# Kernel tuning notes

Measured on AMD Instinct MI355X. Metric: run time of the kernel, lower is better.

## Reference

```python
import jax, jax.numpy as jnp
import numpy as np

B, L, D_MODEL = 2, 1024, 512
N_LAYERS = 4
D_INNER = 2 * D_MODEL          # expand=2
D_STATE = 16
D_CONV = 4
DT_RANK = D_MODEL // 16        # ceil(512/16)=32
EPS = 1e-5


def layernorm(x, w, b):
    m = jnp.mean(x, axis=-1, keepdims=True)
    v = jnp.var(x, axis=-1, keepdims=True)
    return (x - m) * jax.lax.rsqrt(v + EPS) * w + b


def selective_scan(u, delta, A, Bm, Cm, Dp):
    # u, delta: [b,l,d]; Bm, Cm: [b,l,n]; A: [d,n]; Dp: [d]
    def step(h, inp):
        dt_t, b_t, c_t, u_t = inp            # [b,d],[b,n],[b,n],[b,d]
        dA = jnp.exp(dt_t[:, :, None] * A)   # [b,d,n]
        h = dA * h + (dt_t * u_t)[:, :, None] * b_t[:, None, :]
        y = jnp.einsum('bdn,bn->bd', h, c_t)
        return h, y

    b, l, d = u.shape
    n = A.shape[1]
    h0 = jnp.zeros((b, d, n), u.dtype)
    xs = (jnp.swapaxes(delta, 0, 1), jnp.swapaxes(Bm, 0, 1),
          jnp.swapaxes(Cm, 0, 1), jnp.swapaxes(u, 0, 1))
    _, ys = jax.lax.scan(step, h0, xs)       # ys: [l,b,d]
    return jnp.swapaxes(ys, 0, 1) + u * Dp


def mamba(x, in_w, conv_w, conv_b, xp_w, dtp_w, dtp_b, A_log, Dp, out_w):
    # x: [b,l,D_MODEL]
    xz = x @ in_w.T                          # [b,l,2*d_inner]
    xc, z = jnp.split(xz, 2, axis=-1)
    xc = jnp.swapaxes(xc, 1, 2)              # [b,d_inner,l]
    xc = jax.lax.conv_general_dilated(
        xc, conv_w[:, None, :], (1,), [(D_CONV - 1, 0)],
        feature_group_count=D_INNER,
        dimension_numbers=('NCH', 'OIH', 'NCH')) + conv_b[None, :, None]
    xc = jax.nn.silu(jnp.swapaxes(xc, 1, 2))  # [b,l,d_inner]
    x_dbl = xc @ xp_w.T                       # [b,l,dt_rank+2n]
    dt = x_dbl[..., :DT_RANK]
    Bm = x_dbl[..., DT_RANK:DT_RANK + D_STATE]
    Cm = x_dbl[..., DT_RANK + D_STATE:]
    dt = jax.nn.softplus(dt @ dtp_w.T + dtp_b)
    A = -jnp.exp(A_log)
    y = selective_scan(xc, dt, A, Bm, Cm, Dp)
    y = y * jax.nn.silu(z)
    return y @ out_w.T


def forward(x, in_proj_w, conv_w, conv_b, x_proj_w, dt_proj_w, dt_proj_b,
            A_log, D_param, out_proj_w, ln_w, ln_b, fnorm_w, fnorm_b):
    residual = None
    for i in range(in_proj_w.shape[0]):
        residual = x if residual is None else x + residual
        xn = layernorm(x, ln_w[i], ln_b[i])  # norm of incoming x (as in torch src)
        h1 = mamba(xn, in_proj_w[i, 0], conv_w[i, 0], conv_b[i, 0],
                   x_proj_w[i, 0], dt_proj_w[i, 0], dt_proj_b[i, 0],
                   A_log[i, 0], D_param[i, 0], out_proj_w[i, 0])
        h2 = mamba(jnp.flip(xn, axis=1), in_proj_w[i, 1], conv_w[i, 1],
                   conv_b[i, 1], x_proj_w[i, 1], dt_proj_w[i, 1],
                   dt_proj_b[i, 1], A_log[i, 1], D_param[i, 1],
                   out_proj_w[i, 1])
        x = h1 + h2                           # bi_add: NOT flipped back, faithful
    x = x + residual
    return layernorm(x, fnorm_w, fnorm_b)


def setup_inputs() -> dict:
    key = jax.random.key(0)
    ks = jax.random.split(key, 8)
    P2 = (N_LAYERS, 2)
    inp = {}
    inp['x'] = jax.random.normal(ks[0], (B, L, D_MODEL), jnp.float32)
    inp['in_proj_w'] = jax.random.normal(ks[1], P2 + (2 * D_INNER, D_MODEL), jnp.float32) * 0.02
    inp['conv_w'] = jax.random.normal(ks[2], P2 + (D_INNER, D_CONV), jnp.float32) * 0.1
    inp['conv_b'] = jnp.zeros(P2 + (D_INNER,), jnp.float32)
    inp['x_proj_w'] = jax.random.normal(ks[3], P2 + (DT_RANK + 2 * D_STATE, D_INNER), jnp.float32) * 0.02
    inp['dt_proj_w'] = jax.random.normal(ks[4], P2 + (D_INNER, DT_RANK), jnp.float32) * (DT_RANK ** -0.5)
    inp['dt_proj_b'] = jnp.full(P2 + (D_INNER,), float(np.log(np.expm1(0.01))), jnp.float32)
    inp['A_log'] = jnp.broadcast_to(jnp.log(jnp.arange(1, D_STATE + 1, dtype=jnp.float32)), P2 + (D_INNER, D_STATE)).copy()
    inp['D_param'] = jnp.ones(P2 + (D_INNER,), jnp.float32)
    inp['out_proj_w'] = jax.random.normal(ks[5], P2 + (D_MODEL, D_INNER), jnp.float32) * 0.02
    inp['ln_w'] = jnp.ones((N_LAYERS, D_MODEL), jnp.float32)
    inp['ln_b'] = jnp.zeros((N_LAYERS, D_MODEL), jnp.float32)
    inp['fnorm_w'] = jnp.ones((D_MODEL,), jnp.float32)
    inp['fnorm_b'] = jnp.zeros((D_MODEL,), jnp.float32)
    return inp


def reference(x, in_proj_w, conv_w, conv_b, x_proj_w, dt_proj_w, dt_proj_b,
              A_log, D_param, out_proj_w, ln_w, ln_b, fnorm_w, fnorm_b):
    return forward(x, in_proj_w, conv_w, conv_b, x_proj_w, dt_proj_w,
                   dt_proj_b, A_log, D_param, out_proj_w, ln_w, ln_b,
                   fnorm_w, fnorm_b)
```

## Files before the change

kernel.cpp:

```cpp
#include <hip/hip_runtime.h>
#include <hip/hip_bf16.h>
#include <type_traits>

#define B_   2
#define L_   1024
#define DM   512
#define DI   1024
#define DS   16
#define DTR  32
#define ROWS (B_*L_)
#define NCH  16
#define CHUNK (L_/NCH)

#define PO_CW    0
#define PO_CB    32768
#define PO_XPW   40960
#define PO_DTW   565248
#define PO_DTB   827392
#define PO_ALOG  835584
#define PO_DP    966656
#define PO_LNW   974848
#define PO_LNB   976896
#define PO_FNW   978944
#define PO_FNB   979456
#define PO_END   979968

typedef __bf16 bf16x8 __attribute__((ext_vector_type(8)));
typedef float  f32x4  __attribute__((ext_vector_type(4)));
using bf16 = __hip_bfloat16;

__device__ __forceinline__ bf16x8 ld8(const bf16* p){
    return *reinterpret_cast<const bf16x8*>(p);
}
__device__ __forceinline__ float b2f(bf16 v){ return __bfloat162float(v); }

__device__ __forceinline__ void async_cp16(const bf16* g, bf16* s){
    __builtin_amdgcn_global_load_lds(
        (const __attribute__((address_space(1))) unsigned int*)g,
        (__attribute__((address_space(3))) unsigned int*)s, 16, 0, 0);
}

__global__ void detect_kernel(const void* Dp_raw, int* flag){
    *flag = (*(const unsigned int*)Dp_raw == 0x3F800000u) ? 1 : 0;
}

__device__ __forceinline__ bf16 cvload(const void* s, long o, int f){
    return f ? __float2bfloat16(((const float*)s)[o]) : ((const bf16*)s)[o];
}

__global__ void cvt_kernel(const void* src, long off, bf16* dst, int n,
                           const int* flag){
    int i = blockIdx.x*256 + threadIdx.x;
    if (i < n) dst[i] = cvload(src, off + i, *flag);
}

__global__ void cvt_wout_kernel(const void* src, long loff, bf16* dst,
                                const int* flag){
    int i = blockIdx.x*256 + threadIdx.x;
    if (i >= 512*2048) return;
    int n = i >> 11, rest = i & 2047, dir = rest >> 10, d = rest & 1023;
    long o = loff + ((long)dir*512 + n)*1024 + d;
    dst[i] = cvload(src, o, *flag);
}

__global__ void cvt_params_kernel(const void* cw, const void* cb, const void* xpw,
                                  const void* dtw, const void* dtb, const void* al,
                                  const void* dp, const void* lnw, const void* lnb,
                                  const void* fnw, const void* fnb,
                                  bf16* dst, const int* flag){
    int i = blockIdx.x*256 + threadIdx.x;
    if (i >= PO_END) return;
    int f = *flag;
    const void* s; long o;
    if      (i < PO_CB)   { s = cw;  o = i; }
    else if (i < PO_XPW)  { s = cb;  o = i - PO_CB; }
    else if (i < PO_DTW)  { s = xpw; o = i - PO_XPW; }
    else if (i < PO_DTB)  { s = dtw; o = i - PO_DTW; }
    else if (i < PO_ALOG) { s = dtb; o = i - PO_DTB; }
    else if (i < PO_DP)   { s = al;  o = i - PO_ALOG; }
    else if (i < PO_LNW)  { s = dp;  o = i - PO_DP; }
    else if (i < PO_LNB)  { s = lnw; o = i - PO_LNW; }
    else if (i < PO_FNW)  { s = lnb; o = i - PO_LNB; }
    else if (i < PO_FNB)  { s = fnw; o = i - PO_FNW; }
    else                  { s = fnb; o = i - PO_FNB; }
    dst[i] = cvload(s, o, f);
}

__global__ void init_kernel(const void* xin, float* __restrict__ X,
                            float* __restrict__ R, const int* flag){
    size_t i = (size_t)blockIdx.x*256 + threadIdx.x;
    X[i] = *flag ? ((const float*)xin)[i] : b2f(((const bf16*)xin)[i]);
    R[i] = 0.f;
}

__global__ void ln_kernel(const float* __restrict__ X, float* __restrict__ R,
                          const bf16* __restrict__ w, const bf16* __restrict__ b,
                          void* __restrict__ out, int mode, const int* flag){
    int row = blockIdx.x, lane = threadIdx.x;
    size_t base = (size_t)row*DM + lane*8;
    float v[8];
    *(float4*)&v[0] = *(const float4*)(X+base);
    *(float4*)&v[4] = *(const float4*)(X+base+4);
    if (mode == 0){
        float4 r0 = *(const float4*)(R+base);
        float4 r1 = *(const float4*)(R+base+4);
        r0.x += v[0]; r0.y += v[1]; r0.z += v[2]; r0.w += v[3];
        r1.x += v[4]; r1.y += v[5]; r1.z += v[6]; r1.w += v[7];
        *(float4*)(R+base)   = r0;
        *(float4*)(R+base+4) = r1;
    } else {
        float4 r0 = *(const float4*)(R+base);
        float4 r1 = *(const float4*)(R+base+4);
        v[0]+=r0.x; v[1]+=r0.y; v[2]+=r0.z; v[3]+=r0.w;
        v[4]+=r1.x; v[5]+=r1.y; v[6]+=r1.z; v[7]+=r1.w;
    }
    float s=0.f, sq=0.f;
    #pragma unroll
    for (int j=0;j<8;++j){ s += v[j]; sq += v[j]*v[j]; }
    #pragma unroll
    for (int off=32; off>=1; off>>=1){
        s  += __shfl_xor(s,  off, 64);
        sq += __shfl_xor(sq, off, 64);
    }
    float mean = s*(1.f/DM);
    float var  = sq*(1.f/DM) - mean*mean;
    float rs   = rsqrtf(var + 1e-5f);
    bf16x8 wv = ld8(w + lane*8), bv = ld8(b + lane*8);
    float res[8];
    #pragma unroll
    for (int j=0;j<8;++j)
        res[j] = (v[j]-mean)*rs*(float)wv[j] + (float)bv[j];
    if (mode == 1 && *flag){
        float* of = (float*)out;
        *(float4*)(of+base)   = make_float4(res[0],res[1],res[2],res[3]);
        *(float4*)(of+base+4) = make_float4(res[4],res[5],res[6],res[7]);
    } else {
        union { bf16 h[8]; uint4 u; } o;
        #pragma unroll
        for (int j=0;j<8;++j) o.h[j] = __float2bfloat16(res[j]);
        *(uint4*)((bf16*)out + base) = o.u;
    }
}

template<int WM, int WN, int SK, typename CT>
__global__ __launch_bounds__(WM*WN*64)
void gemm_lds(const bf16* __restrict__ A, const bf16* __restrict__ W,
              CT* __restrict__ C, int K, int lda, int ldw, int ldc,
              int selTiles, long wSel){
    constexpr int BM = WM*64, BN = WN*64, T = WM*WN*64;
    constexpr int RA = (BM*4)/T, RB = (BN*4)/T;
    __shared__ __align__(16) bf16 sA[BM*32];
    __shared__ __align__(16) bf16 sB[BN*32];
    int tid = threadIdx.x;
    int mtile = blockIdx.y, ntile = blockIdx.x;
    if (mtile >= selTiles) W += wSel;
    int m0 = mtile*BM, n0 = ntile*BN;
    int kPer = K/SK, kBeg = blockIdx.z*kPer, kEnd = kBeg + kPer;
    if (SK > 1)
        C += (size_t)blockIdx.z * (size_t)(gridDim.y*BM) * (size_t)(gridDim.x*BN);
    int wave = tid>>6, lane = tid&63, quad = lane>>4, r = lane&15;
    int wrow = wave / WN, wcol = wave % WN;
    const bf16* Abase = A + (size_t)m0*lda;
    const bf16* Wbase = W + (size_t)n0*ldw;
    f32x4 acc[4][4] = {};
    for (int k0 = kBeg; k0 < kEnd; k0 += 32){
        #pragma unroll
        for (int rr=0; rr<RA; ++rr){
            int q = rr*T + tid;
            async_cp16(Abase + (size_t)(q>>2)*lda + k0 + (q&3)*8, &sA[q*8]);
        }
        #pragma unroll
        for (int rr=0; rr<RB; ++rr){
            int q = rr*T + tid;
            async_cp16(Wbase + (size_t)(q>>2)*ldw + k0 + (q&3)*8, &sB[q*8]);
        }
        __syncthreads();
        bf16x8 af[4], bw[4];
        #pragma unroll
        for (int mt=0; mt<4; ++mt)
            af[mt] = *(const bf16x8*)&sA[(wrow*64 + mt*16 + r)*32 + quad*8];
        #pragma unroll
        for (int nt=0; nt<4; ++nt)
            bw[nt] = *(const bf16x8*)&sB[(wcol*64 + nt*16 + r)*32 + quad*8];
        #pragma unroll
        for (int mt=0; mt<4; ++mt)
            #pragma unroll
            for (int nt=0; nt<4; ++nt)
                acc[mt][nt] = __builtin_amdgcn_mfma_f32_16x16x32_bf16(
                    af[mt], bw[nt], acc[mt][nt], 0,0,0);
        __syncthreads();
    }
    #pragma unroll
    for (int mt=0; mt<4; ++mt){
        #pragma unroll
        for (int nt=0; nt<4; ++nt){
            int col = n0 + wcol*64 + nt*16 + r;
            #pragma unroll
            for (int ri=0; ri<4; ++ri){
                int row = m0 + wrow*64 + mt*16 + quad*4 + ri;
                size_t idx = (size_t)row*ldc + col;
                if constexpr (std::is_same<CT, bf16>::value)
                    C[idx] = __float2bfloat16(acc[mt][nt][ri]);
                else
                    C[idx] = acc[mt][nt][ri];
            }
        }
    }
}

__global__ void reduce_out(const float* __restrict__ P, float* __restrict__ X){
    int i = blockIdx.x*256 + threadIdx.x;
    X[i] = (P[i] + P[i+1048576]) + (P[i+2097152] + P[i+3145728]);
}

__global__ void reduce_xd(const float* __restrict__ P, float* __restrict__ XD){
    int i = blockIdx.x*256 + threadIdx.x;
    float s = 0.f;
    #pragma unroll
    for (int k=0;k<8;++k) s += P[k*262144 + i];
    int j = i & 63, grow = i >> 6, dir = grow >> 11, row = grow & 2047;
    XD[row*128 + dir*64 + j] = s;
}

__global__ void conv_kernel(const bf16* __restrict__ XZ, const bf16* __restrict__ cw,
                            const bf16* __restrict__ cb, bf16* __restrict__ XC){
    int id  = blockIdx.x*256 + threadIdx.x;
    int d   = id & (DI-1);
    int t   = (id >> 10) & (L_-1);
    int b   = (id >> 20) & 1;
    int dir = id >> 21;
    float wv[4];
    #pragma unroll
    for (int k=0;k<4;++k) wv[k] = b2f(cw[((size_t)dir*DI + d)*4 + k]);
    float acc = b2f(cb[dir*DI + d]);
    #pragma unroll
    for (int k=0;k<4;++k){
        int tau = t - 3 + k;
        if (tau >= 0){
            int sig = dir ? (L_-1-tau) : tau;
            acc += wv[k] * b2f(XZ[((size_t)(b*L_ + sig))*4096 + dir*2048 + d]);
        }
    }
    float s = acc * (1.f/(1.f + __expf(-acc)));
    XC[((size_t)dir*ROWS + (size_t)b*L_ + t)*DI + d] = __float2bfloat16(s);
}

__global__ void dtproj_kernel(const float* __restrict__ XD, const bf16* __restrict__ dtw,
                              const bf16* __restrict__ dtb, bf16* __restrict__ DT){
    int id  = blockIdx.x*256 + threadIdx.x;
    int d   = id & (DI-1);
    int row = (id >> 10) & (ROWS-1);
    int dir = id >> 21;
    const float* xr = XD + (size_t)row*128 + dir*64;
    const bf16*  wp = dtw + ((size_t)dir*DI + d)*DTR;
    float acc = b2f(dtb[dir*DI + d]);
    #pragma unroll
    for (int kk=0;kk<4;++kk){
        bf16x8 wv = ld8(wp + kk*8);
        #pragma unroll
        for (int j=0;j<8;++j) acc += xr[kk*8+j]*(float)wv[j];
    }
    float sp = acc > 20.f ? acc : log1pf(__expf(acc));
    DT[((size_t)dir*ROWS + row)*DI + d] = __float2bfloat16(sp);
}

template<int PHASE>
__global__ __launch_bounds__(256)
void scan_phase(const bf16* __restrict__ DT, const bf16* __restrict__ XC,
                const float* __restrict__ XD, const bf16* __restrict__ XZ,
                const bf16* __restrict__ Al, const bf16* __restrict__ Dp,
                float* __restrict__ SP, float* __restrict__ SH,
                bf16* __restrict__ Y){
    int dirb = blockIdx.z, dir = dirb >> 1, b = dirb & 1;
    int c    = blockIdx.y;
    int d0   = blockIdx.x*128;
    int tid  = threadIdx.x;
    int dl   = tid >> 1, nh = tid & 1;
    int d    = d0 + dl;

    __shared__ bf16  sDT[CHUNK][128];
    __shared__ bf16  sW [CHUNK][128];
    __shared__ float sBC[CHUNK][32];
    __shared__ bf16  sExtra[(PHASE==3) ? CHUNK*128*2 : 2];
    bf16* sG   = &sExtra[0];
    bf16* sUDG = &sExtra[CHUNK*128];

    #pragma unroll
    for (int it=0; it<2; ++it){
        int idx = it*256 + tid;
        int t = idx >> 3, j = idx & 7;
        const float* src = XD + ((size_t)(b*L_) + c*CHUNK + t)*128 + dir*64 + 32 + j*4;
        *(float4*)&sBC[t][j*4] = *(const float4*)src;
    }
    {
        int dcol = tid & 127;
        float Dval = (PHASE==3) ? b2f(Dp[dir*DI + d0 + dcol]) : 0.f;
        #pragma unroll 8
        for (int it=0; it<32; ++it){
            int idx = it*256 + tid;
            int t = idx >> 7;
            int tg = c*CHUNK + t;
            size_t row = (size_t)b*L_ + tg;
            size_t gidx = ((size_t)dir*ROWS + row)*DI + d0 + dcol;
            float dt = b2f(DT[gidx]);
            float u  = b2f(XC[gidx]);
            sDT[t][dcol] = __float2bfloat16(dt);
            sW [t][dcol] = __float2bfloat16(dt*u);
            if (PHASE == 3){
                size_t zrow = dir ? ((size_t)b*L_ + (L_-1-tg)) : row;
                float zv = b2f(XZ[zrow*4096 + dir*2048 + 1024 + d0 + dcol]);
                float g  = zv*(1.f/(1.f + __expf(-zv)));
                sG[t*128 + dcol]   = __float2bfloat16(g);
                sUDG[t*128 + dcol] = __float2bfloat16(u*Dval*g);
            }
        }
    }

    float An[8];
    {
        const bf16* ap = Al + ((size_t)dir*DI + d)*DS + nh*8;
        bf16x8 av = ld8(ap);
        #pragma unroll
        for (int j=0;j<8;++j) An[j] = -__expf((float)av[j]);
    }
    __syncthreads();

    float h[8], pr[8];
    size_t so = ((size_t)(dirb*NCH + c)*DI + d)*DS + nh*8;
    if (PHASE == 3){
        *(f32x4*)&h[0] = *(const f32x4*)&SH[so];
        *(f32x4*)&h[4] = *(const f32x4*)&SH[so+4];
    } else {
        #pragma unroll
        for (int j=0;j<8;++j){ h[j]=0.f; pr[j]=1.f; }
    }

    bf16* Yp = Y + ((size_t)b*L_ + c*CHUNK)*2048 + dir*DI + d;

    for (int tl=0; tl<CHUNK; ++tl){
        float dtv = b2f(sDT[tl][dl]);
        float wv  = b2f(sW [tl][dl]);
        const float* Bp = &sBC[tl][nh*8];
        float y = 0.f;
        #pragma unroll
        for (int j=0;j<8;++j){
            float dA = __expf(dtv*An[j]);
            h[j] = dA*h[j] + wv*Bp[j];
            if (PHASE == 1) pr[j] *= dA;
            else            y += h[j]*Bp[16+j];
        }
        if (PHASE == 3){
            y += __shfl_xor(y, 1, 64);
            if (nh == 0){
                float g   = b2f(sG[tl*128 + dl]);
                float udg = b2f(sUDG[tl*128 + dl]);
                Yp[(size_t)tl*2048] = __float2bfloat16(y*g + udg);
            }
        }
    }
    if (PHASE == 1){
        *(f32x4*)&SP[so]   = *(f32x4*)&pr[0];
        *(f32x4*)&SP[so+4] = *(f32x4*)&pr[4];
        *(f32x4*)&SH[so]   = *(f32x4*)&h[0];
        *(f32x4*)&SH[so+4] = *(f32x4*)&h[4];
    }
}

__global__ void scan_combine(const float* __restrict__ SP, float* __restrict__ SH){
    int id   = blockIdx.x*256 + threadIdx.x;
    int dn   = id & (DI*DS - 1);
    int dirb = id >> 14;
    float hp = 0.f;
    for (int c=0;c<NCH;++c){
        size_t o = ((size_t)(dirb*NCH + c)*DI*DS) + dn;
        float pp = SP[o], he = SH[o];
        float nh = pp*hp + he;
        SH[o] = hp;
        hp = nh;
    }
}

extern "C" void kernel_launch(void* const* d_in, const int* in_sizes, int n_in,
                              void* d_out, int out_size, void* d_ws, size_t ws_size,
                              hipStream_t stream){
    const void* x_raw    = d_in[0];
    const void* inw_raw  = d_in[1];
    const void* convw_raw= d_in[2];
    const void* convb_raw= d_in[3];
    const void* xpw_raw  = d_in[4];
    const void* dtw_raw  = d_in[5];
    const void* dtb_raw  = d_in[6];
    const void* alog_raw = d_in[7];
    const void* dp_raw   = d_in[8];
    const void* outw_raw = d_in[9];
    const void* lnw_raw  = d_in[10];
    const void* lnb_raw  = d_in[11];
    const void* fnw_raw  = d_in[12];
    const void* fnb_raw  = d_in[13];

    char* ws = (char*)d_ws;
    float* X   = (float*)(ws + 0);
    float* R   = (float*)(ws + 4194304);
    bf16*  XN  = (bf16*) (ws + 8388608);
    bf16*  XZ  = (bf16*) (ws + 10485760);
    bf16*  XC  = (bf16*) (ws + 27262976);
    float* XD  = (float*)(ws + 35651584);
    bf16*  DT  = (bf16*) (ws + 36700160);
    bf16*  Y   = (bf16*) (ws + 45088768);
    float* SP  = (float*)(ws + 53477376);
    float* SH  = (float*)(ws + 57671680);
    bf16*  PP  = (bf16*) (ws + 61865984);
    bf16*  WIN = (bf16*) (ws + 63963136);
    bf16*  WOUT= (bf16*) (ws + 68157440);
    int*   FLAG= (int*)  (ws + 70254592);
    float* PX  = (float*)(ws + 45088768);
    float* PO  = (float*)(ws + 27262976);

    detect_kernel<<<1,1,0,stream>>>(dp_raw, FLAG);
    cvt_params_kernel<<<(PO_END+255)/256,256,0,stream>>>(
        convw_raw, convb_raw, xpw_raw, dtw_raw, dtb_raw, alog_raw, dp_raw,
        lnw_raw, lnb_raw, fnw_raw, fnb_raw, PP, FLAG);
    init_kernel<<<4096,256,0,stream>>>(x_raw, X, R, FLAG);

    for (int l=0; l<4; ++l){
        cvt_kernel<<<8192,256,0,stream>>>(inw_raw, (long)l*2097152, WIN, 2097152, FLAG);
        cvt_wout_kernel<<<4096,256,0,stream>>>(outw_raw, (long)l*1048576, WOUT, FLAG);

        ln_kernel<<<ROWS,64,0,stream>>>(X, R, PP+PO_LNW+l*DM, PP+PO_LNB+l*DM, XN, 0, FLAG);

        gemm_lds<2,2,1,bf16><<<dim3(32,16,1),256,0,stream>>>(
            XN, WIN, XZ, 512, 512, 512, 4096, 1<<30, 0);

        conv_kernel<<<16384,256,0,stream>>>(XZ, PP+PO_CW + (size_t)l*2*DI*4,
                                            PP+PO_CB + l*2*DI, XC);

        gemm_lds<2,1,8,float><<<dim3(1,32,8),128,0,stream>>>(
            XC, PP+PO_XPW + (size_t)l*2*64*DI, PX, 1024, 1024, 1024, 64,
            16, (long)64*DI);
        reduce_xd<<<1024,256,0,stream>>>(PX, XD);

        dtproj_kernel<<<16384,256,0,stream>>>(XD, PP+PO_DTW + (size_t)l*2*DI*DTR,
                                              PP+PO_DTB + l*2*DI, DT);

        scan_phase<1><<<dim3(DI/128,NCH,4),256,0,stream>>>(
            DT, XC, XD, XZ, PP+PO_ALOG + (size_t)l*2*DI*DS, PP+PO_DP + l*2*DI,
            SP, SH, Y);
        scan_combine<<<256,256,0,stream>>>(SP, SH);
        scan_phase<3><<<dim3(DI/128,NCH,4),256,0,stream>>>(
            DT, XC, XD, XZ, PP+PO_ALOG + (size_t)l*2*DI*DS, PP+PO_DP + l*2*DI,
            SP, SH, Y);

        gemm_lds<2,2,4,float><<<dim3(4,16,4),256,0,stream>>>(
            Y, WOUT, PO, 2048, 2048, 2048, 512, 1<<30, 0);
        reduce_out<<<4096,256,0,stream>>>(PO, X);
    }

    ln_kernel<<<ROWS,64,0,stream>>>(X, R, PP+PO_FNW, PP+PO_FNB, d_out, 1, FLAG);
}
```

Measured before the change: 773.1 us.

## Merge conversions into one kernel, fold reductions into layernorm, inline scan combine

All weight and input conversions now run in a single upfront kernel that fills full-size per-layer WIN/WOUT buffers, replacing the per-layer conversion launches. The split-K output reduction moves into the layernorm kernel, which reads the four partial sums directly. The separate scan_combine kernel is removed: each phase-3 block rebuilds its carry-in state by walking the earlier chunks' SP/SH values. Scan shared-memory operands are packed as paired bf16 in 32-bit words. The aim is fewer launches and less global traffic, at the cost of a larger workspace and redundant prefix work in later scan chunks.

```diff
diff --git a/kernel.cpp b/kernel.cpp
--- a/kernel.cpp
+++ b/kernel.cpp
@@ -25,6 +25,10 @@
 #define PO_FNB   979456
 #define PO_END   979968
 
+#define N_WIN    (4*2097152)
+#define N_WOUT   (4*1048576)
+#define N_X      1048576
+
 typedef __bf16 bf16x8 __attribute__((ext_vector_type(8)));
 typedef float  f32x4  __attribute__((ext_vector_type(4)));
 using bf16 = __hip_bfloat16;
@@ -33,6 +37,18 @@
     return *reinterpret_cast<const bf16x8*>(p);
 }
 __device__ __forceinline__ float b2f(bf16 v){ return __bfloat162float(v); }
+
+__device__ __forceinline__ unsigned pkbf2(float a, float b){
+    bf16 ha = __float2bfloat16(a), hb = __float2bfloat16(b);
+    unsigned short ua = *(unsigned short*)&ha, ub = *(unsigned short*)&hb;
+    return (unsigned)ua | ((unsigned)ub << 16);
+}
+__device__ __forceinline__ float unpk_lo(unsigned v){
+    unsigned x = v << 16; return __builtin_bit_cast(float, x);
+}
+__device__ __forceinline__ float unpk_hi(unsigned v){
+    unsigned x = v & 0xffff0000u; return __builtin_bit_cast(float, x);
+}
 
 __device__ __forceinline__ void async_cp16(const bf16* g, bf16* s){
     __builtin_amdgcn_global_load_lds(
@@ -48,59 +64,62 @@
     return f ? __float2bfloat16(((const float*)s)[o]) : ((const bf16*)s)[o];
 }
 
-__global__ void cvt_kernel(const void* src, long off, bf16* dst, int n,
-                           const int* flag){
-    int i = blockIdx.x*256 + threadIdx.x;
-    if (i < n) dst[i] = cvload(src, off + i, *flag);
-}
-
-__global__ void cvt_wout_kernel(const void* src, long loff, bf16* dst,
-                                const int* flag){
-    int i = blockIdx.x*256 + threadIdx.x;
-    if (i >= 512*2048) return;
-    int n = i >> 11, rest = i & 2047, dir = rest >> 10, d = rest & 1023;
-    long o = loff + ((long)dir*512 + n)*1024 + d;
-    dst[i] = cvload(src, o, *flag);
-}
-
-__global__ void cvt_params_kernel(const void* cw, const void* cb, const void* xpw,
-                                  const void* dtw, const void* dtb, const void* al,
-                                  const void* dp, const void* lnw, const void* lnb,
-                                  const void* fnw, const void* fnb,
-                                  bf16* dst, const int* flag){
-    int i = blockIdx.x*256 + threadIdx.x;
-    if (i >= PO_END) return;
+__global__ void megacvt_kernel(const void* cw, const void* cb, const void* xpw,
+                               const void* dtw, const void* dtb, const void* al,
+                               const void* dp, const void* lnw, const void* lnb,
+                               const void* fnw, const void* fnb,
+                               const void* inw, const void* outw, const void* xin,
+                               bf16* PP, bf16* WIN, bf16* WOUT,
+                               float* X, float* R, const int* flag){
+    long i = (long)blockIdx.x*256 + threadIdx.x;
     int f = *flag;
-    const void* s; long o;
-    if      (i < PO_CB)   { s = cw;  o = i; }
-    else if (i < PO_XPW)  { s = cb;  o = i - PO_CB; }
-    else if (i < PO_DTW)  { s = xpw; o = i - PO_XPW; }
-    else if (i < PO_DTB)  { s = dtw; o = i - PO_DTW; }
-    else if (i < PO_ALOG) { s = dtb; o = i - PO_DTB; }
-    else if (i < PO_DP)   { s = al;  o = i - PO_ALOG; }
-    else if (i < PO_LNW)  { s = dp;  o = i - PO_DP; }
-    else if (i < PO_LNB)  { s = lnw; o = i - PO_LNW; }
-    else if (i < PO_FNW)  { s = lnb; o = i - PO_LNB; }
-    else if (i < PO_FNB)  { s = fnw; o = i - PO_FNW; }
-    else                  { s = fnb; o = i - PO_FNB; }
-    dst[i] = cvload(s, o, f);
-}
-
-__global__ void init_kernel(const void* xin, float* __restrict__ X,
-                            float* __restrict__ R, const int* flag){
-    size_t i = (size_t)blockIdx.x*256 + threadIdx.x;
-    X[i] = *flag ? ((const float*)xin)[i] : b2f(((const bf16*)xin)[i]);
-    R[i] = 0.f;
-}
-
-__global__ void ln_kernel(const float* __restrict__ X, float* __restrict__ R,
+    if (i < PO_END){
+        const void* s; long o;
+        if      (i < PO_CB)   { s = cw;  o = i; }
+        else if (i < PO_XPW)  { s = cb;  o = i - PO_CB; }
+        else if (i < PO_DTW)  { s = xpw; o = i - PO_XPW; }
+        else if (i < PO_DTB)  { s = dtw; o = i - PO_DTW; }
+        else if (i < PO_ALOG) { s = dtb; o = i - PO_DTB; }
+        else if (i < PO_DP)   { s = al;  o = i - PO_ALOG; }
+        else if (i < PO_LNW)  { s = dp;  o = i - PO_DP; }
+        else if (i < PO_LNB)  { s = lnw; o = i - PO_LNW; }
+        else if (i < PO_FNW)  { s = lnb; o = i - PO_LNB; }
+        else if (i < PO_FNB)  { s = fnw; o = i - PO_FNW; }
+        else                  { s = fnb; o = i - PO_FNB; }
+        PP[i] = cvload(s, o, f);
+        return;
+    }
+    i -= PO_END;
+    if (i < N_WIN){ WIN[i] = cvload(inw, i, f); return; }
+    i -= N_WIN;
+    if (i < N_WOUT){
+        long l = i >> 20, r = i & 1048575;
+        long n = r >> 11, dir = (r >> 10) & 1, d = r & 1023;
+        WOUT[i] = cvload(outw, ((l*2 + dir)*512 + n)*1024 + d, f);
+        return;
+    }
+    i -= N_WOUT;
+    if (i < N_X){
+        X[i] = f ? ((const float*)xin)[i] : b2f(((const bf16*)xin)[i]);
+        R[i] = 0.f;
+    }
+}
+
+__global__ void ln_kernel(const float* __restrict__ P, int nparts,
+                          float* __restrict__ R,
                           const bf16* __restrict__ w, const bf16* __restrict__ b,
                           void* __restrict__ out, int mode, const int* flag){
     int row = blockIdx.x, lane = threadIdx.x;
     size_t base = (size_t)row*DM + lane*8;
     float v[8];
-    *(float4*)&v[0] = *(const float4*)(X+base);
-    *(float4*)&v[4] = *(const float4*)(X+base+4);
+    *(float4*)&v[0] = *(const float4*)(P+base);
+    *(float4*)&v[4] = *(const float4*)(P+base+4);
+    for (int k=1; k<nparts; ++k){
+        float4 a0 = *(const float4*)(P + (size_t)k*1048576 + base);
+        float4 a1 = *(const float4*)(P + (size_t)k*1048576 + base + 4);
+        v[0]+=a0.x; v[1]+=a0.y; v[2]+=a0.z; v[3]+=a0.w;
+        v[4]+=a1.x; v[5]+=a1.y; v[6]+=a1.z; v[7]+=a1.w;
+    }
     if (mode == 0){
         float4 r0 = *(const float4*)(R+base);
         float4 r1 = *(const float4*)(R+base+4);
@@ -208,11 +227,6 @@
     }
 }
 
-__global__ void reduce_out(const float* __restrict__ P, float* __restrict__ X){
-    int i = blockIdx.x*256 + threadIdx.x;
-    X[i] = (P[i] + P[i+1048576]) + (P[i+2097152] + P[i+3145728]);
-}
-
 __global__ void reduce_xd(const float* __restrict__ P, float* __restrict__ XD){
     int i = blockIdx.x*256 + threadIdx.x;
     float s = 0.f;
@@ -278,12 +292,9 @@
     int dl   = tid >> 1, nh = tid & 1;
     int d    = d0 + dl;
 
-    __shared__ bf16  sDT[CHUNK][128];
-    __shared__ bf16  sW [CHUNK][128];
+    __shared__ unsigned sDTW[CHUNK][128];
     __shared__ float sBC[CHUNK][32];
-    __shared__ bf16  sExtra[(PHASE==3) ? CHUNK*128*2 : 2];
-    bf16* sG   = &sExtra[0];
-    bf16* sUDG = &sExtra[CHUNK*128];
+    __shared__ unsigned sGU[(PHASE==3) ? CHUNK*128 : 1];
 
     #pragma unroll
     for (int it=0; it<2; ++it){
@@ -304,14 +315,12 @@
             size_t gidx = ((size_t)dir*ROWS + row)*DI + d0 + dcol;
             float dt = b2f(DT[gidx]);
             float u  = b2f(XC[gidx]);
-            sDT[t][dcol] = __float2bfloat16(dt);
-            sW [t][dcol] = __float2bfloat16(dt*u);
+            sDTW[t][dcol] = pkbf2(dt, dt*u);
             if (PHASE == 3){
                 size_t zrow = dir ? ((size_t)b*L_ + (L_-1-tg)) : row;
                 float zv = b2f(XZ[zrow*4096 + dir*2048 + 1024 + d0 + dcol]);
                 float g  = zv*(1.f/(1.f + __expf(-zv)));
-                sG[t*128 + dcol]   = __float2bfloat16(g);
-                sUDG[t*128 + dcol] = __float2bfloat16(u*Dval*g);
+                sGU[t*128 + dcol] = pkbf2(g, u*Dval*g);
             }
         }
     }
@@ -323,23 +332,32 @@
         #pragma unroll
         for (int j=0;j<8;++j) An[j] = -__expf((float)av[j]);
     }
-    __syncthreads();
 
     float h[8], pr[8];
     size_t so = ((size_t)(dirb*NCH + c)*DI + d)*DS + nh*8;
+    #pragma unroll
+    for (int j=0;j<8;++j){ h[j]=0.f; pr[j]=1.f; }
     if (PHASE == 3){
-        *(f32x4*)&h[0] = *(const f32x4*)&SH[so];
-        *(f32x4*)&h[4] = *(const f32x4*)&SH[so+4];
-    } else {
-        #pragma unroll
-        for (int j=0;j<8;++j){ h[j]=0.f; pr[j]=1.f; }
-    }
+        for (int cc=0; cc<c; ++cc){
+            size_t o = ((size_t)(dirb*NCH + cc)*DI + d)*DS + nh*8;
+            f32x4 p0 = *(const f32x4*)&SP[o];
+            f32x4 p1 = *(const f32x4*)&SP[o+4];
+            f32x4 h0 = *(const f32x4*)&SH[o];
+            f32x4 h1 = *(const f32x4*)&SH[o+4];
+            #pragma unroll
+            for (int j=0;j<4;++j){
+                h[j]   = p0[j]*h[j]   + h0[j];
+                h[4+j] = p1[j]*h[4+j] + h1[j];
+            }
+        }
+    }
+    __syncthreads();
 
     bf16* Yp = Y + ((size_t)b*L_ + c*CHUNK)*2048 + dir*DI + d;
 
     for (int tl=0; tl<CHUNK; ++tl){
-        float dtv = b2f(sDT[tl][dl]);
-        float wv  = b2f(sW [tl][dl]);
+        unsigned dw = sDTW[tl][dl];
+        float dtv = unpk_lo(dw), wv = unpk_hi(dw);
         const float* Bp = &sBC[tl][nh*8];
         float y = 0.f;
         #pragma unroll
@@ -352,9 +370,8 @@
         if (PHASE == 3){
             y += __shfl_xor(y, 1, 64);
             if (nh == 0){
-                float g   = b2f(sG[tl*128 + dl]);
-                float udg = b2f(sUDG[tl*128 + dl]);
-                Yp[(size_t)tl*2048] = __float2bfloat16(y*g + udg);
+                unsigned gu = sGU[tl*128 + dl];
+                Yp[(size_t)tl*2048] = __float2bfloat16(y*unpk_lo(gu) + unpk_hi(gu));
             }
         }
     }
@@ -363,20 +380,6 @@
         *(f32x4*)&SP[so+4] = *(f32x4*)&pr[4];
         *(f32x4*)&SH[so]   = *(f32x4*)&h[0];
         *(f32x4*)&SH[so+4] = *(f32x4*)&h[4];
-    }
-}
-
-__global__ void scan_combine(const float* __restrict__ SP, float* __restrict__ SH){
-    int id   = blockIdx.x*256 + threadIdx.x;
-    int dn   = id & (DI*DS - 1);
-    int dirb = id >> 14;
-    float hp = 0.f;
-    for (int c=0;c<NCH;++c){
-        size_t o = ((size_t)(dirb*NCH + c)*DI*DS) + dn;
-        float pp = SP[o], he = SH[o];
-        float nh = pp*hp + he;
-        SH[o] = hp;
-        hp = nh;
     }
 }
 
@@ -406,30 +409,32 @@
     bf16*  XC  = (bf16*) (ws + 27262976);
     float* XD  = (float*)(ws + 35651584);
     bf16*  DT  = (bf16*) (ws + 36700160);
-    bf16*  Y   = (bf16*) (ws + 45088768);
-    float* SP  = (float*)(ws + 53477376);
-    float* SH  = (float*)(ws + 57671680);
-    bf16*  PP  = (bf16*) (ws + 61865984);
-    bf16*  WIN = (bf16*) (ws + 63963136);
-    bf16*  WOUT= (bf16*) (ws + 68157440);
-    int*   FLAG= (int*)  (ws + 70254592);
-    float* PX  = (float*)(ws + 45088768);
-    float* PO  = (float*)(ws + 27262976);
+    bf16*  Y   = (bf16*) (ws + 44040192);
+    float* SP  = (float*)(ws + 52428800);
+    float* SH  = (float*)(ws + 56623104);
+    bf16*  PP  = (bf16*) (ws + 60817408);
+    bf16*  WIN = (bf16*) (ws + 62914560);
+    bf16*  WOUT= (bf16*) (ws + 79691776);
+    float* PX  = (float*)(ws + 88080384);
+    float* PO  = (float*)(ws + 96468992);
+    int*   FLAG= (int*)  (ws + 113246208);
 
     detect_kernel<<<1,1,0,stream>>>(dp_raw, FLAG);
-    cvt_params_kernel<<<(PO_END+255)/256,256,0,stream>>>(
-        convw_raw, convb_raw, xpw_raw, dtw_raw, dtb_raw, alog_raw, dp_raw,
-        lnw_raw, lnb_raw, fnw_raw, fnb_raw, PP, FLAG);
-    init_kernel<<<4096,256,0,stream>>>(x_raw, X, R, FLAG);
+    {
+        long total = (long)PO_END + N_WIN + N_WOUT + N_X;
+        int blocks = (int)((total + 255)/256);
+        megacvt_kernel<<<blocks,256,0,stream>>>(
+            convw_raw, convb_raw, xpw_raw, dtw_raw, dtb_raw, alog_raw, dp_raw,
+            lnw_raw, lnb_raw, fnw_raw, fnb_raw, inw_raw, outw_raw, x_raw,
+            PP, WIN, WOUT, X, R, FLAG);
+    }
 
     for (int l=0; l<4; ++l){
-        cvt_kernel<<<8192,256,0,stream>>>(inw_raw, (long)l*2097152, WIN, 2097152, FLAG);
-        cvt_wout_kernel<<<4096,256,0,stream>>>(outw_raw, (long)l*1048576, WOUT, FLAG);
-
-        ln_kernel<<<ROWS,64,0,stream>>>(X, R, PP+PO_LNW+l*DM, PP+PO_LNB+l*DM, XN, 0, FLAG);
+        ln_kernel<<<ROWS,64,0,stream>>>(l==0 ? X : PO, l==0 ? 1 : 4, R,
+                                        PP+PO_LNW+l*DM, PP+PO_LNB+l*DM, XN, 0, FLAG);
 
         gemm_lds<2,2,1,bf16><<<dim3(32,16,1),256,0,stream>>>(
-            XN, WIN, XZ, 512, 512, 512, 4096, 1<<30, 0);
+            XN, WIN + (size_t)l*2097152, XZ, 512, 512, 512, 4096, 1<<30, 0);
 
         conv_kernel<<<16384,256,0,stream>>>(XZ, PP+PO_CW + (size_t)l*2*DI*4,
                                             PP+PO_CB + l*2*DI, XC);
@@ -445,15 +450,13 @@
         scan_phase<1><<<dim3(DI/128,NCH,4),256,0,stream>>>(
             DT, XC, XD, XZ, PP+PO_ALOG + (size_t)l*2*DI*DS, PP+PO_DP + l*2*DI,
             SP, SH, Y);
-        scan_combine<<<256,256,0,stream>>>(SP, SH);
         scan_phase<3><<<dim3(DI/128,NCH,4),256,0,stream>>>(
             DT, XC, XD, XZ, PP+PO_ALOG + (size_t)l*2*DI*DS, PP+PO_DP + l*2*DI,
             SP, SH, Y);
 
         gemm_lds<2,2,4,float><<<dim3(4,16,4),256,0,stream>>>(
-            Y, WOUT, PO, 2048, 2048, 2048, 512, 1<<30, 0);
-        reduce_out<<<4096,256,0,stream>>>(PO, X);
-    }
-
-    ln_kernel<<<ROWS,64,0,stream>>>(X, R, PP+PO_FNW, PP+PO_FNB, d_out, 1, FLAG);
-}
+            Y, WOUT + (size_t)l*1048576, PO, 2048, 2048, 2048, 512, 1<<30, 0);
+    }
+
+    ln_kernel<<<ROWS,64,0,stream>>>(PO, 4, R, PP+PO_FNW, PP+PO_FNB, d_out, 1, FLAG);
+}
```

Result: faster. 742.7 us (-3.9%).
